# Performance work log

Measured on AMD Instinct MI355X. Metric: run time of the kernel, lower is better.

## Reference

```python
import jax, jax.numpy as jnp
import numpy as np

B, T, D, H = 8, 2048, 1024, 128

def setup_inputs() -> dict:
    key = jax.random.key(0)
    ks = jax.random.split(key, 8)
    s = 1.0 / np.sqrt(D)
    return {
        "x": jax.random.normal(ks[0], (B, T, D), dtype=jnp.float32),
        "att": jax.random.normal(ks[1], (B, T, D), dtype=jnp.float32),
        "Wk": jax.random.uniform(ks[2], (D, H), minval=-s, maxval=s, dtype=jnp.float32),
        "bk": jax.random.uniform(ks[3], (H,), minval=-s, maxval=s, dtype=jnp.float32),
        "Wq": jax.random.uniform(ks[4], (D, H), minval=-s, maxval=s, dtype=jnp.float32),
        "bq": jax.random.uniform(ks[5], (H,), minval=-s, maxval=s, dtype=jnp.float32),
        "Wv": jax.random.uniform(ks[6], (D, H), minval=-s, maxval=s, dtype=jnp.float32),
        "bv": jax.random.uniform(ks[7], (H,), minval=-s, maxval=s, dtype=jnp.float32),
    }

def reference(x, att, Wk, bk, Wq, bq, Wv, bv):
    # k, q from `att`; v from `x` (as in the original module)
    k = jnp.einsum('btd,dh->bth', att, Wk) + bk   # [B,T,H]
    q = jnp.einsum('btd,dh->bth', att, Wq) + bq   # [B,T,H]
    v = jnp.einsum('btd,dh->bth', x, Wv) + bv     # [B,T,H]
    # Faithful to source: scores / head_size**(-0.5) == scores * sqrt(head_size)
    scale = jnp.asarray(k.shape[-1], jnp.float32) ** 0.5
    scores = jnp.einsum('bqh,bkh->bqk', q, k) * scale  # [B,T,T]
    att_mat = jax.nn.softmax(scores, axis=-1)
    # dropout p=0.0 -> identity (eval semantics)
    return jnp.einsum('bqk,bkh->bqh', att_mat, v)      # [B,T,H]
```

## Files before the change

### kernel.cpp

```cpp
#include <hip/hip_runtime.h>
#include <stdint.h>

typedef unsigned short u16;
typedef __attribute__((ext_vector_type(8))) short bf16x8;
typedef __attribute__((ext_vector_type(4))) float f32x4;

#define T_LEN 2048
#define D_DIM 1024
#define H_DIM 128
#define SCALE_LOG2 16.32223116f

#define EXP2F(x) __builtin_amdgcn_exp2f(x)

__device__ __forceinline__ u16 f2bf(float f) {
  uint32_t u = __float_as_uint(f);
  u += 0x7FFFu + ((u >> 16) & 1u);
  return (u16)(u >> 16);
}
__device__ __forceinline__ float bf2f(u16 h) { return __uint_as_float(((uint32_t)h) << 16); }

__device__ __forceinline__ void gload16(const void* g, void* l) {
  __builtin_amdgcn_global_load_lds(
      (const __attribute__((address_space(1))) uint32_t*)(uintptr_t)g,
      (__attribute__((address_space(3))) uint32_t*)(uint32_t)(uintptr_t)l,
      16, 0, 0);
}

#define VMCNT0() asm volatile("s_waitcnt vmcnt(0)" ::: "memory")
#define VMLG0() asm volatile("s_waitcnt vmcnt(0) lgkmcnt(0)" ::: "memory")
#define BAR() __builtin_amdgcn_s_barrier()

#define MFMA(a, b, c) __builtin_amdgcn_mfma_f32_16x16x32_bf16((a), (b), (c), 0, 0, 0)

__global__ __launch_bounds__(256) void prep_w(
    const float* __restrict__ Wk, const float* __restrict__ Wq, const float* __restrict__ Wv,
    u16* __restrict__ wqh, u16* __restrict__ wql,
    u16* __restrict__ wkh, u16* __restrict__ wkl,
    u16* __restrict__ wvh) {
  __shared__ u16 th[3][128][16];
  __shared__ u16 tl[2][128][16];
  const int i = threadIdx.x;
  const int d0 = blockIdx.x * 16;
  const int dl = i >> 4;
  const int hb = (i & 15) * 8;
  const int d = d0 + dl;
#pragma unroll
  for (int e = 0; e < 8; ++e) {
    int h = hb + e;
    float q = Wq[d * H_DIM + h] * SCALE_LOG2;
    float k = Wk[d * H_DIM + h];
    float v = Wv[d * H_DIM + h];
    u16 qh = f2bf(q); th[0][h][dl] = qh; tl[0][h][dl] = f2bf(q - bf2f(qh));
    u16 kh = f2bf(k); th[1][h][dl] = kh; tl[1][h][dl] = f2bf(k - bf2f(kh));
    th[2][h][dl] = f2bf(v);
  }
  __syncthreads();
  const int h = i >> 1, c = i & 1;
  u16* planes[5] = {wqh, wql, wkh, wkl, wvh};
  const u16* srcs[5] = {&th[0][0][0], &tl[0][0][0], &th[1][0][0], &tl[1][0][0], &th[2][0][0]};
#pragma unroll
  for (int p = 0; p < 5; ++p) {
    bf16x8 v8 = *(const bf16x8*)(srcs[p] + h * 16 + c * 8);
    *(bf16x8*)(planes[p] + h * 1024 + d0 + c * 8) = v8;
  }
}

#define QBUF 53248

__global__ __launch_bounds__(256) void qkv_proj(
    const float* __restrict__ att, const float* __restrict__ x,
    const u16* __restrict__ wqh, const u16* __restrict__ wql,
    const u16* __restrict__ wkh, const u16* __restrict__ wkl,
    const u16* __restrict__ wvh,
    const float* __restrict__ bq, const float* __restrict__ bk, const float* __restrict__ bv,
    u16* __restrict__ qhp, u16* __restrict__ qlp,
    u16* __restrict__ khp, u16* __restrict__ klp,
    u16* __restrict__ vtp) {
  __shared__ __attribute__((aligned(128))) char lds[104 * 1024];

  const int tid = threadIdx.x;
  const int wid = tid >> 6;
  const int ln = tid & 63;
  const int g = ln >> 4;
  const int cl = ln & 15;
  const int t0g = blockIdx.x * 64;

  const f32x4 fz = {0.f, 0.f, 0.f, 0.f};
  f32x4 accq[2][4], acck[2][4], accv[2][4];
#pragma unroll
  for (int a = 0; a < 2; ++a)
#pragma unroll
    for (int s = 0; s < 4; ++s) { accq[a][s] = fz; acck[a][s] = fz; accv[a][s] = fz; }

  const int arow = tid >> 2;
  const int ac = tid & 3;
  const float* attp = att + (size_t)(t0g + arow) * D_DIM + ac * 8;
  const float* xp   = x   + (size_t)(t0g + arow) * D_DIM + ac * 8;
  const int aw_off = arow * 64 + ((ac ^ ((arow >> 1) & 3)) * 16);

  auto STAGE_W = [&](int b, int ks) {
    char* wt = lds + b * QBUF + 12288;
#pragma unroll
    for (int j = 0; j < 10; ++j) {
      int seg = wid * 10 + j;
      int p = seg >> 3;
      int s = seg & 7;
      int db = s * 1024 + ln * 16;
      int row = db >> 6;
      int c = (db >> 4) & 3;
      int cs = c ^ ((row >> 1) & 3);
      const u16* wp = (p == 0) ? wqh : (p == 1) ? wql : (p == 2) ? wkh : (p == 3) ? wkl : wvh;
      gload16(wp + row * 1024 + ks * 32 + cs * 8, wt + p * 8192 + s * 1024);
    }
  };
  auto CWRITE_A = [&](int b, f32x4 f0, f32x4 f1, f32x4 g0, f32x4 g1) {
    bf16x8 vh, vl, vx;
#pragma unroll
    for (int e = 0; e < 4; ++e) {
      u16 h0 = f2bf(f0[e]); vh[e] = (short)h0; vl[e] = (short)f2bf(f0[e] - bf2f(h0));
      u16 h1 = f2bf(f1[e]); vh[e + 4] = (short)h1; vl[e + 4] = (short)f2bf(f1[e] - bf2f(h1));
      vx[e] = (short)f2bf(g0[e]); vx[e + 4] = (short)f2bf(g1[e]);
    }
    char* dst = lds + b * QBUF + aw_off;
    *(bf16x8*)dst = vh;
    *(bf16x8*)(dst + 4096) = vl;
    *(bf16x8*)(dst + 8192) = vx;
  };

  {
    f32x4 f0 = *(const f32x4*)(attp);
    f32x4 f1 = *(const f32x4*)(attp + 4);
    f32x4 g0 = *(const f32x4*)(xp);
    f32x4 g1 = *(const f32x4*)(xp + 4);
    STAGE_W(0, 0);
    CWRITE_A(0, f0, f1, g0, g1);
  }
  VMLG0();
  BAR();

  int cur = 0;
  for (int ks = 0; ks < 32; ++ks) {
    f32x4 pf0, pf1, pg0, pg1;
    if (ks < 31) {
      pf0 = *(const f32x4*)(attp + (ks + 1) * 32);
      pf1 = *(const f32x4*)(attp + (ks + 1) * 32 + 4);
      pg0 = *(const f32x4*)(xp + (ks + 1) * 32);
      pg1 = *(const f32x4*)(xp + (ks + 1) * 32 + 4);
      STAGE_W(cur ^ 1, ks + 1);
    }
    char* base = lds + cur * QBUF;
    char* aAh = base;
    char* aAl = base + 4096;
    char* aXh = base + 8192;
    char* wt  = base + 12288;
    bf16x8 ah[4], al[4], xh[4];
#pragma unroll
    for (int s = 0; s < 4; ++s) {
      int row = s * 16 + cl;
      int byte = row * 64 + ((g ^ ((row >> 1) & 3)) * 16);
      ah[s] = *(const bf16x8*)(aAh + byte);
      al[s] = *(const bf16x8*)(aAl + byte);
      xh[s] = *(const bf16x8*)(aXh + byte);
    }
#pragma unroll
    for (int lnt = 0; lnt < 2; ++lnt) {
      int hrow = (2 * wid + lnt) * 16 + cl;
      int wb = hrow * 64 + ((g ^ ((hrow >> 1) & 3)) * 16);
      bf16x8 bqh_ = *(const bf16x8*)(wt + 0 * 8192 + wb);
      bf16x8 bql_ = *(const bf16x8*)(wt + 1 * 8192 + wb);
      bf16x8 bkh_ = *(const bf16x8*)(wt + 2 * 8192 + wb);
      bf16x8 bkl_ = *(const bf16x8*)(wt + 3 * 8192 + wb);
      bf16x8 bvh_ = *(const bf16x8*)(wt + 4 * 8192 + wb);
#pragma unroll
      for (int s = 0; s < 4; ++s) {
        accq[lnt][s] = MFMA(ah[s], bqh_, accq[lnt][s]);
        accq[lnt][s] = MFMA(al[s], bqh_, accq[lnt][s]);
        accq[lnt][s] = MFMA(ah[s], bql_, accq[lnt][s]);
        acck[lnt][s] = MFMA(ah[s], bkh_, acck[lnt][s]);
        acck[lnt][s] = MFMA(al[s], bkh_, acck[lnt][s]);
        acck[lnt][s] = MFMA(ah[s], bkl_, acck[lnt][s]);
        accv[lnt][s] = MFMA(xh[s], bvh_, accv[lnt][s]);
      }
    }
    if (ks < 31) CWRITE_A(cur ^ 1, pf0, pf1, pg0, pg1);
    VMLG0();
    BAR();
    cur ^= 1;
  }

  char* vbuf = lds;
#pragma unroll
  for (int lnt = 0; lnt < 2; ++lnt) {
    int h = (2 * wid + lnt) * 16 + cl;
    float bqv = bq[h] * SCALE_LOG2, bkv = bk[h], bvv = bv[h];
#pragma unroll
    for (int s = 0; s < 4; ++s) {
#pragma unroll
      for (int r = 0; r < 4; ++r) {
        int t = s * 16 + g * 4 + r;
        size_t idx = (size_t)(t0g + t) * H_DIM + h;
        float qv = accq[lnt][s][r] + bqv;
        u16 qh_ = f2bf(qv);
        qhp[idx] = qh_;
        qlp[idx] = f2bf(qv - bf2f(qh_));
        float kv = acck[lnt][s][r] + bkv;
        u16 kh_ = f2bf(kv);
        khp[idx] = kh_;
        klp[idx] = f2bf(kv - bf2f(kh_));
        float vv = accv[lnt][s][r] + bvv;
        int c3 = t >> 3;
        int byte = h * 128 + ((c3 ^ (h & 7)) * 16) + (t & 7) * 2;
        *(u16*)(vbuf + byte) = f2bf(vv);
      }
    }
  }
  __syncthreads();
  {
    int h = tid >> 1, half = tid & 1;
    int b_ = t0g >> 11;
    int tb = t0g & 2047;
    u16* dst = vtp + ((size_t)(b_ * H_DIM + h)) * T_LEN + tb + half * 32;
#pragma unroll
    for (int c2 = 0; c2 < 4; ++c2) {
      int c3 = half * 4 + c2;
      bf16x8 v8 = *(const bf16x8*)(vbuf + h * 128 + ((c3 ^ (h & 7)) * 16));
      *(bf16x8*)(dst + c2 * 8) = v8;
    }
  }
}

#define ABUF 49152

__global__ __launch_bounds__(256) void attn(
    const u16* __restrict__ qhp, const u16* __restrict__ qlp,
    const u16* __restrict__ khp, const u16* __restrict__ klp,
    const u16* __restrict__ vtp,
    float* __restrict__ out) {
  __shared__ __attribute__((aligned(128))) char lds[104 * 1024];
  char* pB = lds + 96 * 1024;

  const int tid = threadIdx.x;
  const int wid = tid >> 6;
  const int ln = tid & 63;
  const int g = ln >> 4;
  const int cl = ln & 15;
  const int bid = blockIdx.x;
  const int b_ = bid & 7;
  const int t0 = (bid >> 3) * 64;
  char* pW = pB + wid * 2048;

  auto STAGE = [&](int b, int tk) {
    char* kH = lds + b * ABUF;
    char* kL = kH + 16384;
    char* vT = kH + 32768;
#pragma unroll
    for (int j = 0; j < 4; ++j) {
      int s = wid * 4 + j;
      int db = s * 1024 + ln * 16;
      int row = db >> 8;
      int c16 = (db >> 4) & 15;
      int cs = c16 ^ (row & 7);
      size_t gidx = (size_t)(b_ * T_LEN + tk + row) * H_DIM + cs * 8;
      gload16(khp + gidx, kH + s * 1024);
      gload16(klp + gidx, kL + s * 1024);
      int vrow = db >> 7;
      int c3 = (db >> 4) & 7;
      int vcs = c3 ^ (vrow & 7);
      size_t vidx = (size_t)(b_ * H_DIM + vrow) * T_LEN + tk + vcs * 8;
      gload16(vtp + vidx, vT + s * 1024);
    }
  };

  bf16x8 qh_f[4], ql_f[4];
  {
    size_t qrow = (size_t)(b_ * T_LEN + t0 + wid * 16 + cl) * H_DIM;
#pragma unroll
    for (int kc = 0; kc < 4; ++kc) {
      qh_f[kc] = *(const bf16x8*)(qhp + qrow + kc * 32 + g * 8);
      ql_f[kc] = *(const bf16x8*)(qlp + qrow + kc * 32 + g * 8);
    }
  }
  const f32x4 fz = {0.f, 0.f, 0.f, 0.f};
  float m_[4] = {-1e30f, -1e30f, -1e30f, -1e30f};
  float l_[4] = {0.f, 0.f, 0.f, 0.f};
  f32x4 o_[8];
#pragma unroll
  for (int ht = 0; ht < 8; ++ht) o_[ht] = fz;

  STAGE(0, 0);
  VMCNT0();
  BAR();

  int cur = 0;
  for (int kv = 0; kv < 32; ++kv) {
    if (kv < 31) STAGE(cur ^ 1, (kv + 1) * 64);

    char* kH = lds + cur * ABUF;
    char* kL = kH + 16384;
    char* vT = kH + 32768;
    f32x4 sc[4];
#pragma unroll
    for (int nt = 0; nt < 4; ++nt) sc[nt] = fz;
#pragma unroll
    for (int kc = 0; kc < 4; ++kc) {
#pragma unroll
      for (int nt = 0; nt < 4; ++nt) {
        int row = nt * 16 + cl;
        int byte = row * 256 + (((kc * 4 + g) ^ (row & 7)) * 16);
        bf16x8 bh = *(const bf16x8*)(kH + byte);
        bf16x8 bl = *(const bf16x8*)(kL + byte);
        sc[nt] = MFMA(qh_f[kc], bh, sc[nt]);
        sc[nt] = MFMA(ql_f[kc], bh, sc[nt]);
        sc[nt] = MFMA(qh_f[kc], bl, sc[nt]);
      }
    }
    float sfv[4];
#pragma unroll
    for (int r = 0; r < 4; ++r) {
      float pm = fmaxf(fmaxf(sc[0][r], sc[1][r]), fmaxf(sc[2][r], sc[3][r]));
#pragma unroll
      for (int d = 1; d < 16; d <<= 1) pm = fmaxf(pm, __shfl_xor(pm, d));
      float mn = fmaxf(m_[r], pm);
      float sf = EXP2F(m_[r] - mn);
      m_[r] = mn; sfv[r] = sf;
      float ps = 0.f;
      int prow = g * 4 + r;
#pragma unroll
      for (int nt = 0; nt < 4; ++nt) {
        float p = EXP2F(sc[nt][r] - mn);
        ps += p;
        int c3 = nt * 2 + (cl >> 3);
        int byte = prow * 128 + ((c3 ^ (prow & 7)) * 16) + (cl & 7) * 2;
        *(u16*)(pW + byte) = f2bf(p);
      }
#pragma unroll
      for (int d = 1; d < 16; d <<= 1) ps += __shfl_xor(ps, d);
      l_[r] = l_[r] * sf + ps;
    }
#pragma unroll
    for (int ht = 0; ht < 8; ++ht) {
      o_[ht][0] *= sfv[0]; o_[ht][1] *= sfv[1]; o_[ht][2] *= sfv[2]; o_[ht][3] *= sfv[3];
    }
#pragma unroll
    for (int kc2 = 0; kc2 < 2; ++kc2) {
      int pbyte = cl * 128 + (((kc2 * 4 + g) ^ (cl & 7)) * 16);
      bf16x8 ap = *(const bf16x8*)(pW + pbyte);
#pragma unroll
      for (int ht = 0; ht < 8; ++ht) {
        int vrow = ht * 16 + cl;
        int vbyte = vrow * 128 + (((kc2 * 4 + g) ^ (vrow & 7)) * 16);
        bf16x8 bv_ = *(const bf16x8*)(vT + vbyte);
        o_[ht] = MFMA(ap, bv_, o_[ht]);
      }
    }
    VMCNT0();
    BAR();
    cur ^= 1;
  }
  float inv[4];
#pragma unroll
  for (int r = 0; r < 4; ++r) inv[r] = 1.f / l_[r];
  size_t obase = (size_t)(b_ * T_LEN + t0 + wid * 16) * H_DIM;
#pragma unroll
  for (int r = 0; r < 4; ++r) {
#pragma unroll
    for (int ht = 0; ht < 8; ++ht) {
      out[obase + (size_t)(g * 4 + r) * H_DIM + ht * 16 + cl] = o_[ht][r] * inv[r];
    }
  }
}

extern "C" void kernel_launch(void* const* d_in, const int* in_sizes, int n_in,
                              void* d_out, int out_size, void* d_ws, size_t ws_size,
                              hipStream_t stream) {
  const float* x   = (const float*)d_in[0];
  const float* att = (const float*)d_in[1];
  const float* Wk  = (const float*)d_in[2];
  const float* bk  = (const float*)d_in[3];
  const float* Wq  = (const float*)d_in[4];
  const float* bq  = (const float*)d_in[5];
  const float* Wv  = (const float*)d_in[6];
  const float* bv  = (const float*)d_in[7];
  float* out = (float*)d_out;
  char* ws = (char*)d_ws;

  u16* wqh = (u16*)(ws);
  u16* wql = (u16*)(ws + 256 * 1024);
  u16* wkh = (u16*)(ws + 512 * 1024);
  u16* wkl = (u16*)(ws + 768 * 1024);
  u16* wvh = (u16*)(ws + 1024 * 1024);
  u16* qhp = (u16*)(ws + (size_t)2 * 1024 * 1024);
  u16* qlp = (u16*)(ws + (size_t)6 * 1024 * 1024);
  u16* khp = (u16*)(ws + (size_t)10 * 1024 * 1024);
  u16* klp = (u16*)(ws + (size_t)14 * 1024 * 1024);
  u16* vtp = (u16*)(ws + (size_t)18 * 1024 * 1024);

  prep_w<<<64, 256, 0, stream>>>(Wk, Wq, Wv, wqh, wql, wkh, wkl, wvh);
  qkv_proj<<<256, 256, 0, stream>>>(att, x, wqh, wql, wkh, wkl, wvh,
                                    bq, bk, bv, qhp, qlp, khp, klp, vtp);
  attn<<<256, 256, 0, stream>>>(qhp, qlp, khp, klp, vtp, out);
}
```

Measured before the change: 265.2 us.

## Double waves per block with split-KV attention and s_setprio around MFMA

Both qkv_proj and attn now launch 512 threads per block. In qkv_proj, each wave computes one 16-column head tile instead of two, and the att and x staging is split between the two thread halves. In attn, two wave groups each process half of the KV sequence in 32-row chunks with their own double buffers, then merge their partial softmax state (max, sum, output) through LDS. s_setprio is raised around MFMA bursts. The aim is more waves per CU to hide latency, at the cost of a merge step, smaller per-iteration tiles and more barriers.

```diff
diff --git a/kernel.cpp b/kernel.cpp
--- a/kernel.cpp
+++ b/kernel.cpp
@@ -29,6 +29,7 @@
 #define VMCNT0() asm volatile("s_waitcnt vmcnt(0)" ::: "memory")
 #define VMLG0() asm volatile("s_waitcnt vmcnt(0) lgkmcnt(0)" ::: "memory")
 #define BAR() __builtin_amdgcn_s_barrier()
+#define PRIO(n) __builtin_amdgcn_s_setprio(n)
 
 #define MFMA(a, b, c) __builtin_amdgcn_mfma_f32_16x16x32_bf16((a), (b), (c), 0, 0, 0)
 
@@ -67,7 +68,7 @@
 
 #define QBUF 53248
 
-__global__ __launch_bounds__(256) void qkv_proj(
+__global__ __launch_bounds__(512) void qkv_proj(
     const float* __restrict__ att, const float* __restrict__ x,
     const u16* __restrict__ wqh, const u16* __restrict__ wql,
     const u16* __restrict__ wkh, const u16* __restrict__ wkl,
@@ -86,23 +87,22 @@
   const int t0g = blockIdx.x * 64;
 
   const f32x4 fz = {0.f, 0.f, 0.f, 0.f};
-  f32x4 accq[2][4], acck[2][4], accv[2][4];
-#pragma unroll
-  for (int a = 0; a < 2; ++a)
-#pragma unroll
-    for (int s = 0; s < 4; ++s) { accq[a][s] = fz; acck[a][s] = fz; accv[a][s] = fz; }
-
-  const int arow = tid >> 2;
-  const int ac = tid & 3;
-  const float* attp = att + (size_t)(t0g + arow) * D_DIM + ac * 8;
-  const float* xp   = x   + (size_t)(t0g + arow) * D_DIM + ac * 8;
-  const int aw_off = arow * 64 + ((ac ^ ((arow >> 1) & 3)) * 16);
+  f32x4 accq[4], acck[4], accv[4];
+#pragma unroll
+  for (int s = 0; s < 4; ++s) { accq[s] = fz; acck[s] = fz; accv[s] = fz; }
+
+  const int isA = tid < 256;
+  const int at = tid & 255;
+  const int arow = at >> 2;
+  const int ac = at & 3;
+  const float* srcp = (isA ? att : x) + (size_t)(t0g + arow) * D_DIM + ac * 8;
+  const int aw_off = (isA ? 0 : 8192) + arow * 64 + ((ac ^ ((arow >> 1) & 3)) * 16);
 
   auto STAGE_W = [&](int b, int ks) {
     char* wt = lds + b * QBUF + 12288;
 #pragma unroll
-    for (int j = 0; j < 10; ++j) {
-      int seg = wid * 10 + j;
+    for (int j = 0; j < 5; ++j) {
+      int seg = wid * 5 + j;
       int p = seg >> 3;
       int s = seg & 7;
       int db = s * 1024 + ln * 16;
@@ -113,85 +113,76 @@
       gload16(wp + row * 1024 + ks * 32 + cs * 8, wt + p * 8192 + s * 1024);
     }
   };
-  auto CWRITE_A = [&](int b, f32x4 f0, f32x4 f1, f32x4 g0, f32x4 g1) {
-    bf16x8 vh, vl, vx;
+  auto CWRITE_A = [&](int b, f32x4 f0, f32x4 f1) {
+    bf16x8 vh, vl;
 #pragma unroll
     for (int e = 0; e < 4; ++e) {
       u16 h0 = f2bf(f0[e]); vh[e] = (short)h0; vl[e] = (short)f2bf(f0[e] - bf2f(h0));
       u16 h1 = f2bf(f1[e]); vh[e + 4] = (short)h1; vl[e + 4] = (short)f2bf(f1[e] - bf2f(h1));
-      vx[e] = (short)f2bf(g0[e]); vx[e + 4] = (short)f2bf(g1[e]);
     }
     char* dst = lds + b * QBUF + aw_off;
     *(bf16x8*)dst = vh;
-    *(bf16x8*)(dst + 4096) = vl;
-    *(bf16x8*)(dst + 8192) = vx;
+    if (isA) *(bf16x8*)(dst + 4096) = vl;
   };
 
   {
-    f32x4 f0 = *(const f32x4*)(attp);
-    f32x4 f1 = *(const f32x4*)(attp + 4);
-    f32x4 g0 = *(const f32x4*)(xp);
-    f32x4 g1 = *(const f32x4*)(xp + 4);
+    f32x4 f0 = *(const f32x4*)(srcp);
+    f32x4 f1 = *(const f32x4*)(srcp + 4);
     STAGE_W(0, 0);
-    CWRITE_A(0, f0, f1, g0, g1);
+    CWRITE_A(0, f0, f1);
   }
   VMLG0();
   BAR();
 
   int cur = 0;
   for (int ks = 0; ks < 32; ++ks) {
-    f32x4 pf0, pf1, pg0, pg1;
+    f32x4 pf0, pf1;
     if (ks < 31) {
-      pf0 = *(const f32x4*)(attp + (ks + 1) * 32);
-      pf1 = *(const f32x4*)(attp + (ks + 1) * 32 + 4);
-      pg0 = *(const f32x4*)(xp + (ks + 1) * 32);
-      pg1 = *(const f32x4*)(xp + (ks + 1) * 32 + 4);
+      pf0 = *(const f32x4*)(srcp + (ks + 1) * 32);
+      pf1 = *(const f32x4*)(srcp + (ks + 1) * 32 + 4);
       STAGE_W(cur ^ 1, ks + 1);
     }
     char* base = lds + cur * QBUF;
-    char* aAh = base;
-    char* aAl = base + 4096;
-    char* aXh = base + 8192;
-    char* wt  = base + 12288;
+    char* wt = base + 12288;
     bf16x8 ah[4], al[4], xh[4];
 #pragma unroll
     for (int s = 0; s < 4; ++s) {
       int row = s * 16 + cl;
       int byte = row * 64 + ((g ^ ((row >> 1) & 3)) * 16);
-      ah[s] = *(const bf16x8*)(aAh + byte);
-      al[s] = *(const bf16x8*)(aAl + byte);
-      xh[s] = *(const bf16x8*)(aXh + byte);
-    }
-#pragma unroll
-    for (int lnt = 0; lnt < 2; ++lnt) {
-      int hrow = (2 * wid + lnt) * 16 + cl;
+      ah[s] = *(const bf16x8*)(base + byte);
+      al[s] = *(const bf16x8*)(base + 4096 + byte);
+      xh[s] = *(const bf16x8*)(base + 8192 + byte);
+    }
+    {
+      int hrow = wid * 16 + cl;
       int wb = hrow * 64 + ((g ^ ((hrow >> 1) & 3)) * 16);
       bf16x8 bqh_ = *(const bf16x8*)(wt + 0 * 8192 + wb);
       bf16x8 bql_ = *(const bf16x8*)(wt + 1 * 8192 + wb);
       bf16x8 bkh_ = *(const bf16x8*)(wt + 2 * 8192 + wb);
       bf16x8 bkl_ = *(const bf16x8*)(wt + 3 * 8192 + wb);
       bf16x8 bvh_ = *(const bf16x8*)(wt + 4 * 8192 + wb);
+      PRIO(1);
 #pragma unroll
       for (int s = 0; s < 4; ++s) {
-        accq[lnt][s] = MFMA(ah[s], bqh_, accq[lnt][s]);
-        accq[lnt][s] = MFMA(al[s], bqh_, accq[lnt][s]);
-        accq[lnt][s] = MFMA(ah[s], bql_, accq[lnt][s]);
-        acck[lnt][s] = MFMA(ah[s], bkh_, acck[lnt][s]);
-        acck[lnt][s] = MFMA(al[s], bkh_, acck[lnt][s]);
-        acck[lnt][s] = MFMA(ah[s], bkl_, acck[lnt][s]);
-        accv[lnt][s] = MFMA(xh[s], bvh_, accv[lnt][s]);
-      }
-    }
-    if (ks < 31) CWRITE_A(cur ^ 1, pf0, pf1, pg0, pg1);
+        accq[s] = MFMA(ah[s], bqh_, accq[s]);
+        accq[s] = MFMA(al[s], bqh_, accq[s]);
+        accq[s] = MFMA(ah[s], bql_, accq[s]);
+        acck[s] = MFMA(ah[s], bkh_, acck[s]);
+        acck[s] = MFMA(al[s], bkh_, acck[s]);
+        acck[s] = MFMA(ah[s], bkl_, acck[s]);
+        accv[s] = MFMA(xh[s], bvh_, accv[s]);
+      }
+      PRIO(0);
+    }
+    if (ks < 31) CWRITE_A(cur ^ 1, pf0, pf1);
     VMLG0();
     BAR();
     cur ^= 1;
   }
 
   char* vbuf = lds;
-#pragma unroll
-  for (int lnt = 0; lnt < 2; ++lnt) {
-    int h = (2 * wid + lnt) * 16 + cl;
+  {
+    int h = wid * 16 + cl;
     float bqv = bq[h] * SCALE_LOG2, bkv = bk[h], bvv = bv[h];
 #pragma unroll
     for (int s = 0; s < 4; ++s) {
@@ -199,15 +190,15 @@
       for (int r = 0; r < 4; ++r) {
         int t = s * 16 + g * 4 + r;
         size_t idx = (size_t)(t0g + t) * H_DIM + h;
-        float qv = accq[lnt][s][r] + bqv;
+        float qv = accq[s][r] + bqv;
         u16 qh_ = f2bf(qv);
         qhp[idx] = qh_;
         qlp[idx] = f2bf(qv - bf2f(qh_));
-        float kv = acck[lnt][s][r] + bkv;
+        float kv = acck[s][r] + bkv;
         u16 kh_ = f2bf(kv);
         khp[idx] = kh_;
         klp[idx] = f2bf(kv - bf2f(kh_));
-        float vv = accv[lnt][s][r] + bvv;
+        float vv = accv[s][r] + bvv;
         int c3 = t >> 3;
         int byte = h * 128 + ((c3 ^ (h & 7)) * 16) + (t & 7) * 2;
         *(u16*)(vbuf + byte) = f2bf(vv);
@@ -216,64 +207,69 @@
   }
   __syncthreads();
   {
-    int h = tid >> 1, half = tid & 1;
-    int b_ = t0g >> 11;
+    int h = tid >> 2, qtr = tid & 3;
+    int b2 = t0g >> 11;
     int tb = t0g & 2047;
-    u16* dst = vtp + ((size_t)(b_ * H_DIM + h)) * T_LEN + tb + half * 32;
-#pragma unroll
-    for (int c2 = 0; c2 < 4; ++c2) {
-      int c3 = half * 4 + c2;
+    u16* dst = vtp + ((size_t)(b2 * H_DIM + h)) * T_LEN + tb + qtr * 16;
+#pragma unroll
+    for (int c2 = 0; c2 < 2; ++c2) {
+      int c3 = qtr * 2 + c2;
       bf16x8 v8 = *(const bf16x8*)(vbuf + h * 128 + ((c3 ^ (h & 7)) * 16));
       *(bf16x8*)(dst + c2 * 8) = v8;
     }
   }
 }
 
-#define ABUF 49152
-
-__global__ __launch_bounds__(256) void attn(
+#define KVB 32
+#define GBUF 24576
+
+__global__ __launch_bounds__(512) void attn(
     const u16* __restrict__ qhp, const u16* __restrict__ qlp,
     const u16* __restrict__ khp, const u16* __restrict__ klp,
     const u16* __restrict__ vtp,
     float* __restrict__ out) {
   __shared__ __attribute__((aligned(128))) char lds[104 * 1024];
-  char* pB = lds + 96 * 1024;
 
   const int tid = threadIdx.x;
   const int wid = tid >> 6;
+  const int w4 = wid & 3;
+  const int gb = wid >> 2;
   const int ln = tid & 63;
   const int g = ln >> 4;
   const int cl = ln & 15;
   const int bid = blockIdx.x;
   const int b_ = bid & 7;
   const int t0 = (bid >> 3) * 64;
-  char* pW = pB + wid * 2048;
-
-  auto STAGE = [&](int b, int tk) {
-    char* kH = lds + b * ABUF;
-    char* kL = kH + 16384;
-    char* vT = kH + 32768;
-#pragma unroll
-    for (int j = 0; j < 4; ++j) {
-      int s = wid * 4 + j;
+  char* gl = lds + gb * 2 * GBUF;
+  char* pW = lds + 96 * 1024 + wid * 1024;
+
+  auto STAGE = [&](int cb, int tk) {
+    char* base = gl + cb * GBUF;
+#pragma unroll
+    for (int j = 0; j < 6; ++j) {
+      int seg = w4 * 6 + j;
+      int p = seg >> 3;
+      int s = seg & 7;
       int db = s * 1024 + ln * 16;
-      int row = db >> 8;
-      int c16 = (db >> 4) & 15;
-      int cs = c16 ^ (row & 7);
-      size_t gidx = (size_t)(b_ * T_LEN + tk + row) * H_DIM + cs * 8;
-      gload16(khp + gidx, kH + s * 1024);
-      gload16(klp + gidx, kL + s * 1024);
-      int vrow = db >> 7;
-      int c3 = (db >> 4) & 7;
-      int vcs = c3 ^ (vrow & 7);
-      size_t vidx = (size_t)(b_ * H_DIM + vrow) * T_LEN + tk + vcs * 8;
-      gload16(vtp + vidx, vT + s * 1024);
+      if (p < 2) {
+        int row = db >> 8;
+        int c16 = (db >> 4) & 15;
+        int cs = c16 ^ (row & 7);
+        size_t gidx = (size_t)(b_ * T_LEN + tk + row) * H_DIM + cs * 8;
+        gload16((p ? klp : khp) + gidx, base + p * 8192 + s * 1024);
+      } else {
+        int vrow = db >> 6;
+        int c = (db >> 4) & 3;
+        int vcs = c ^ (vrow & 3);
+        size_t vidx = (size_t)(b_ * H_DIM + vrow) * T_LEN + tk + vcs * 8;
+        gload16(vtp + vidx, base + 16384 + s * 1024);
+      }
     }
   };
 
   bf16x8 qh_f[4], ql_f[4];
   {
-    size_t qrow = (size_t)(b_ * T_LEN + t0 + wid * 16 + cl) * H_DIM;
+    size_t qrow = (size_t)(b_ * T_LEN + t0 + w4 * 16 + cl) * H_DIM;
 #pragma unroll
     for (int kc = 0; kc < 4; ++kc) {
       qh_f[kc] = *(const bf16x8*)(qhp + qrow + kc * 32 + g * 8);
@@ -287,24 +283,25 @@
 #pragma unroll
   for (int ht = 0; ht < 8; ++ht) o_[ht] = fz;
 
-  STAGE(0, 0);
+  const int tkbase = gb * 1024;
+
+  STAGE(0, tkbase);
   VMCNT0();
   BAR();
 
   int cur = 0;
   for (int kv = 0; kv < 32; ++kv) {
-    if (kv < 31) STAGE(cur ^ 1, (kv + 1) * 64);
-
-    char* kH = lds + cur * ABUF;
-    char* kL = kH + 16384;
-    char* vT = kH + 32768;
-    f32x4 sc[4];
-#pragma unroll
-    for (int nt = 0; nt < 4; ++nt) sc[nt] = fz;
+    if (kv < 31) STAGE(cur ^ 1, tkbase + (kv + 1) * KVB);
+
+    char* kH = gl + cur * GBUF;
+    char* kL = kH + 8192;
+    char* vT = kH + 16384;
+    f32x4 sc[2] = {fz, fz};
+    PRIO(1);
 #pragma unroll
     for (int kc = 0; kc < 4; ++kc) {
 #pragma unroll
-      for (int nt = 0; nt < 4; ++nt) {
+      for (int nt = 0; nt < 2; ++nt) {
         int row = nt * 16 + cl;
         int byte = row * 256 + (((kc * 4 + g) ^ (row & 7)) * 16);
         bf16x8 bh = *(const bf16x8*)(kH + byte);
@@ -314,10 +311,11 @@
         sc[nt] = MFMA(qh_f[kc], bl, sc[nt]);
       }
     }
+    PRIO(0);
     float sfv[4];
 #pragma unroll
     for (int r = 0; r < 4; ++r) {
-      float pm = fmaxf(fmaxf(sc[0][r], sc[1][r]), fmaxf(sc[2][r], sc[3][r]));
+      float pm = fmaxf(sc[0][r], sc[1][r]);
 #pragma unroll
       for (int d = 1; d < 16; d <<= 1) pm = fmaxf(pm, __shfl_xor(pm, d));
       float mn = fmaxf(m_[r], pm);
@@ -326,11 +324,11 @@
       float ps = 0.f;
       int prow = g * 4 + r;
 #pragma unroll
-      for (int nt = 0; nt < 4; ++nt) {
+      for (int nt = 0; nt < 2; ++nt) {
         float p = EXP2F(sc[nt][r] - mn);
         ps += p;
         int c3 = nt * 2 + (cl >> 3);
-        int byte = prow * 128 + ((c3 ^ (prow & 7)) * 16) + (cl & 7) * 2;
+        int byte = prow * 64 + ((c3 ^ (prow & 3)) * 16) + (cl & 7) * 2;
         *(u16*)(pW + byte) = f2bf(p);
       }
 #pragma unroll
@@ -341,31 +339,59 @@
     for (int ht = 0; ht < 8; ++ht) {
       o_[ht][0] *= sfv[0]; o_[ht][1] *= sfv[1]; o_[ht][2] *= sfv[2]; o_[ht][3] *= sfv[3];
     }
-#pragma unroll
-    for (int kc2 = 0; kc2 < 2; ++kc2) {
-      int pbyte = cl * 128 + (((kc2 * 4 + g) ^ (cl & 7)) * 16);
+    {
+      int pbyte = cl * 64 + ((g ^ (cl & 3)) * 16);
       bf16x8 ap = *(const bf16x8*)(pW + pbyte);
+      PRIO(1);
 #pragma unroll
       for (int ht = 0; ht < 8; ++ht) {
         int vrow = ht * 16 + cl;
-        int vbyte = vrow * 128 + (((kc2 * 4 + g) ^ (vrow & 7)) * 16);
+        int vbyte = vrow * 64 + ((g ^ (vrow & 3)) * 16);
         bf16x8 bv_ = *(const bf16x8*)(vT + vbyte);
         o_[ht] = MFMA(ap, bv_, o_[ht]);
       }
+      PRIO(0);
     }
     VMCNT0();
     BAR();
     cur ^= 1;
   }
-  float inv[4];
-#pragma unroll
-  for (int r = 0; r < 4; ++r) inv[r] = 1.f / l_[r];
-  size_t obase = (size_t)(b_ * T_LEN + t0 + wid * 16) * H_DIM;
-#pragma unroll
-  for (int r = 0; r < 4; ++r) {
+
+  if (gb == 1) {
+    char* ob = lds + w4 * 8192 + ln * 128;
+#pragma unroll
+    for (int ht = 0; ht < 8; ++ht) *(f32x4*)(ob + ht * 16) = o_[ht];
+    f32x4 mv = {m_[0], m_[1], m_[2], m_[3]};
+    f32x4 lv = {l_[0], l_[1], l_[2], l_[3]};
+    char* mb = lds + 32768 + w4 * 2048 + ln * 32;
+    *(f32x4*)mb = mv;
+    *(f32x4*)(mb + 16) = lv;
+  }
+  __syncthreads();
+  if (gb == 0) {
+    char* ob = lds + w4 * 8192 + ln * 128;
+    char* mb = lds + 32768 + w4 * 2048 + ln * 32;
+    f32x4 mB = *(const f32x4*)mb;
+    f32x4 lB = *(const f32x4*)(mb + 16);
+    float sA[4], sB[4];
+#pragma unroll
+    for (int r = 0; r < 4; ++r) {
+      float m = fmaxf(m_[r], mB[r]);
+      float fa = EXP2F(m_[r] - m);
+      float fb = EXP2F(mB[r] - m);
+      float inv = 1.f / (l_[r] * fa + lB[r] * fb);
+      sA[r] = fa * inv;
+      sB[r] = fb * inv;
+    }
+    size_t obase = (size_t)(b_ * T_LEN + t0 + w4 * 16) * H_DIM;
 #pragma unroll
     for (int ht = 0; ht < 8; ++ht) {
-      out[obase + (size_t)(g * 4 + r) * H_DIM + ht * 16 + cl] = o_[ht][r] * inv[r];
+      f32x4 oB = *(const f32x4*)(ob + ht * 16);
+#pragma unroll
+      for (int r = 0; r < 4; ++r) {
+        out[obase + (size_t)(g * 4 + r) * H_DIM + ht * 16 + cl] =
+            o_[ht][r] * sA[r] + oB[r] * sB[r];
+      }
     }
   }
 }
@@ -396,7 +422,7 @@
   u16* vtp = (u16*)(ws + (size_t)18 * 1024 * 1024);
 
   prep_w<<<64, 256, 0, stream>>>(Wk, Wq, Wv, wqh, wql, wkh, wkl, wvh);
-  qkv_proj<<<256, 256, 0, stream>>>(att, x, wqh, wql, wkh, wkl, wvh,
+  qkv_proj<<<256, 512, 0, stream>>>(att, x, wqh, wql, wkh, wkl, wvh,
                                     bq, bk, bv, qhp, qlp, khp, klp, vtp);
-  attn<<<256, 256, 0, stream>>>(qhp, qlp, khp, klp, vtp, out);
-}
+  attn<<<256, 512, 0, stream>>>(qhp, qlp, khp, klp, vtp, out);
+}
```

Result: no change. 262.1 us (-1.2%).
